# Kernel tuning notes

Hardware: AMD Instinct MI355X
Metric: run time of the kernel (lower is better)

The kernel has to match this reference:

```python
import jax, jax.numpy as jnp
import numpy as np

B, N, D_IN, D_SC, C, H, W = 32, 512, 256, 32, 48, 152, 160


def setup_inputs() -> dict:
    key = jax.random.key(0)
    k1, k2, k3, k4 = jax.random.split(key, 4)
    spatial_info = jax.random.normal(k1, (B, C, H, W), dtype=jnp.float32)
    entity_embeddings = jax.random.normal(k2, (B, N, D_IN), dtype=jnp.float32)
    entity_mask = jnp.ones((B, N), dtype=jnp.float32)
    locations = jax.random.randint(k3, (B, N, 2), 0, 152).astype(jnp.int64)
    W_proj = jax.random.normal(k4, (D_IN, D_SC), dtype=jnp.float32) / np.sqrt(D_IN)
    b_proj = jnp.zeros((D_SC,), dtype=jnp.float32)
    return {"spatial_info": spatial_info, "entity_embeddings": entity_embeddings,
            "entity_mask": entity_mask, "locations": locations,
            "W_proj": W_proj, "b_proj": b_proj}


def reference(spatial_info, entity_embeddings, entity_mask, locations, W_proj, b_proj):
    # fc_block: linear + ReLU projection of entity embeddings -> [B, N, D_SC]
    proj = jax.nn.relu(jnp.einsum('bnd,de->bne', entity_embeddings, W_proj) + b_proj)
    proj = proj * entity_mask[:, :, None]

    # build flat spatial indices (clamped), with per-batch bias  -> [B*N]
    y = jnp.clip(locations[..., 0], 0, H - 1)
    x = jnp.clip(locations[..., 1], 0, W - 1)
    flat = y * W + x                                   # [B, N]
    bias = (jnp.arange(B, dtype=flat.dtype) * (H * W))[:, None]
    idx = (flat + bias).reshape(-1)                    # [B*N]

    # scatter-add projected embeddings onto dense grid [B*H*W, D_SC]
    vals = proj.reshape(B * N, D_SC)
    scatter_map = jnp.zeros((B * H * W, D_SC), dtype=proj.dtype).at[idx].add(vals)
    scatter_map = scatter_map.reshape(B, H, W, D_SC).transpose(0, 3, 1, 2)  # [B, D_SC, H, W]

    return jnp.concatenate([spatial_info, scatter_map], axis=1)
```

## Files before the change

kernel.cpp:

```cpp
#include <hip/hip_runtime.h>

#define Bsz  32
#define Nn   512
#define DIN  256
#define DSC  32
#define Cc   48
#define Hh   152
#define Ww   160
#define HW   (Hh * Ww)
#define COUT (Cc + DSC)
#define HALF (HW / 2)
#define HP4  (HALF / 4)

#define CP_N4     (Bsz * Cc * (HW / 4))
#define CP_GRID   2048
#define CP_THREAD 256
#define CP_STRIDE (CP_GRID * CP_THREAD)
#define SLAB4     (Cc * (HW / 4))
#define SC4       ((COUT - Cc) * (HW / 4))
#define PR_GRID   ((Bsz * Nn) / 32)

typedef float f4 __attribute__((ext_vector_type(4)));

__global__ __launch_bounds__(CP_THREAD, 4) void proj_copy_kernel(
    const float* __restrict__ spatial, const float* __restrict__ emb,
    const float* __restrict__ mask, const int* __restrict__ loc,
    const float* __restrict__ Wp, const float* __restrict__ bp,
    float* __restrict__ out, float* __restrict__ projws,
    int* __restrict__ idxws) {

    __shared__ float Ws[DIN][DSC];

    const int bid = blockIdx.x;
    const int tid = threadIdx.x;

    if (bid >= PR_GRID) {
        const f4* __restrict__ src = (const f4*)spatial;
        f4* __restrict__       dst = (f4*)out;
        unsigned i = (bid - PR_GRID) * CP_THREAD + tid;
        #pragma unroll 1
        for (int k = 0; k < 4; ++k) {
            const unsigned i0 = i, i1 = i + CP_STRIDE,
                           i2 = i + 2 * CP_STRIDE, i3 = i + 3 * CP_STRIDE;
            const f4 a0 = src[i0];
            const f4 a1 = src[i1];
            const f4 a2 = src[i2];
            const f4 a3 = src[i3];
            __builtin_nontemporal_store(a0, dst + i0 + (i0 / (unsigned)SLAB4) * SC4);
            __builtin_nontemporal_store(a1, dst + i1 + (i1 / (unsigned)SLAB4) * SC4);
            __builtin_nontemporal_store(a2, dst + i2 + (i2 / (unsigned)SLAB4) * SC4);
            __builtin_nontemporal_store(a3, dst + i3 + (i3 / (unsigned)SLAB4) * SC4);
            i += 4 * CP_STRIDE;
        }
        {
            const f4 a = src[i];
            __builtin_nontemporal_store(a, dst + i + (i / (unsigned)SLAB4) * SC4);
            i += CP_STRIDE;
        }
        if (i < (unsigned)CP_N4) {
            const f4 a = src[i];
            __builtin_nontemporal_store(a, dst + i + (i / (unsigned)SLAB4) * SC4);
        }
        return;
    }

    const int ent0 = bid * 32;

    for (int i = tid; i < (DIN * DSC) / 4; i += 256)
        ((f4*)Ws)[i] = ((const f4*)Wp)[i];
    __syncthreads();

    const int g   = tid >> 3;
    const int dq  = (tid & 7) * 4;
    const int ent = ent0 + g;

    const f4* __restrict__ erow = (const f4*)(emb + (size_t)ent * DIN);

    float ax = bp[dq + 0], ay = bp[dq + 1], az = bp[dq + 2], aw = bp[dq + 3];

    #pragma unroll 4
    for (int k4 = 0; k4 < DIN / 4; ++k4) {
        const f4 ev = erow[k4];
        const int k = k4 * 4;
        const f4 w0 = *(const f4*)&Ws[k + 0][dq];
        const f4 w1 = *(const f4*)&Ws[k + 1][dq];
        const f4 w2 = *(const f4*)&Ws[k + 2][dq];
        const f4 w3 = *(const f4*)&Ws[k + 3][dq];
        ax = fmaf(ev.x, w0.x, fmaf(ev.y, w1.x, fmaf(ev.z, w2.x, fmaf(ev.w, w3.x, ax))));
        ay = fmaf(ev.x, w0.y, fmaf(ev.y, w1.y, fmaf(ev.z, w2.y, fmaf(ev.w, w3.y, ay))));
        az = fmaf(ev.x, w0.z, fmaf(ev.y, w1.z, fmaf(ev.z, w2.z, fmaf(ev.w, w3.z, az))));
        aw = fmaf(ev.x, w0.w, fmaf(ev.y, w1.w, fmaf(ev.z, w2.w, fmaf(ev.w, w3.w, aw))));
    }

    const float m = mask[ent];
    f4 r;
    r.x = fmaxf(ax, 0.f) * m;
    r.y = fmaxf(ay, 0.f) * m;
    r.z = fmaxf(az, 0.f) * m;
    r.w = fmaxf(aw, 0.f) * m;
    ((f4*)projws)[(size_t)ent * (DSC / 4) + (tid & 7)] = r;

    if ((tid & 7) == 0) {
        int y = loc[2 * ent + 0];
        int x = loc[2 * ent + 1];
        y = min(max(y, 0), Hh - 1);
        x = min(max(x, 0), Ww - 1);
        idxws[ent] = y * Ww + x;
    }
}

__global__ __launch_bounds__(256) void gather_kernel(
    const float* __restrict__ projws, const int* __restrict__ idxws,
    float* __restrict__ out) {

    __shared__ float facc[HALF];

    const int g    = blockIdx.x;
    const int b    = g >> 6;
    const int c    = (g >> 1) & 31;
    const int lo   = (g & 1) * HALF;
    const int tid  = threadIdx.x;

    for (int i = tid; i < HP4; i += 256) ((f4*)facc)[i] = (f4)(0.f);
    __syncthreads();

    const int2 v = ((const int2*)(idxws + b * Nn))[tid];
    {
        const int r0 = v.x - lo;
        if ((unsigned)r0 < (unsigned)HALF) {
            const float p = projws[((size_t)b * Nn + 2 * tid) * DSC + c];
            if (p != 0.f) atomicAdd(&facc[r0], p);
        }
        const int r1 = v.y - lo;
        if ((unsigned)r1 < (unsigned)HALF) {
            const float p = projws[((size_t)b * Nn + 2 * tid + 1) * DSC + c];
            if (p != 0.f) atomicAdd(&facc[r1], p);
        }
    }
    __syncthreads();

    f4* obase = (f4*)(out + ((size_t)(b * COUT + Cc + c)) * HW + lo);
    for (int i = tid; i < HP4; i += 256)
        __builtin_nontemporal_store(((const f4*)facc)[i], obase + i);
}

__global__ __launch_bounds__(256) void init_out_kernel(
    const float* __restrict__ spatial, float* __restrict__ out) {
    const int plane = blockIdx.x;
    const int b = plane / COUT;
    const int c = plane % COUT;
    f4* dst = (f4*)(out + (size_t)plane * HW);
    if (c < Cc) {
        const f4* src = (const f4*)(spatial + ((size_t)b * Cc + c) * HW);
        for (int i = threadIdx.x; i < HW / 4; i += blockDim.x) dst[i] = src[i];
    } else {
        for (int i = threadIdx.x; i < HW / 4; i += blockDim.x) dst[i] = (f4)(0.f);
    }
}

__global__ __launch_bounds__(256) void scatter_kernel(
    const float* __restrict__ emb, const float* __restrict__ mask,
    const int* __restrict__ loc, const float* __restrict__ Wp,
    const float* __restrict__ bp, float* __restrict__ out) {

    __shared__ float Ws[DIN][DSC];
    __shared__ float Es[32][DIN + 4];

    const int tid  = threadIdx.x;
    const int ent0 = blockIdx.x * 32;

    for (int i = tid; i < (DIN * DSC) / 4; i += 256)
        ((f4*)Ws)[i] = ((const f4*)Wp)[i];
    for (int i = tid; i < (32 * DIN) / 4; i += 256) {
        const int e  = i >> 6;
        const int k4 = i & 63;
        *(f4*)&Es[e][k4 * 4] =
            ((const f4*)(emb + (size_t)(ent0 + e) * DIN))[k4];
    }
    __syncthreads();

    const int g   = tid >> 3;
    const int dq  = (tid & 7) * 4;
    const int ent = ent0 + g;
    const int b   = ent >> 9;

    float ax = bp[dq + 0], ay = bp[dq + 1], az = bp[dq + 2], aw = bp[dq + 3];

    #pragma unroll 4
    for (int k = 0; k < DIN; k += 4) {
        const f4 ev = *(const f4*)&Es[g][k];
        const f4 w0 = *(const f4*)&Ws[k + 0][dq];
        const f4 w1 = *(const f4*)&Ws[k + 1][dq];
        const f4 w2 = *(const f4*)&Ws[k + 2][dq];
        const f4 w3 = *(const f4*)&Ws[k + 3][dq];
        ax = fmaf(ev.x, w0.x, fmaf(ev.y, w1.x, fmaf(ev.z, w2.x, fmaf(ev.w, w3.x, ax))));
        ay = fmaf(ev.x, w0.y, fmaf(ev.y, w1.y, fmaf(ev.z, w2.y, fmaf(ev.w, w3.y, ay))));
        az = fmaf(ev.x, w0.z, fmaf(ev.y, w1.z, fmaf(ev.z, w2.z, fmaf(ev.w, w3.z, az))));
        aw = fmaf(ev.x, w0.w, fmaf(ev.y, w1.w, fmaf(ev.z, w2.w, fmaf(ev.w, w3.w, aw))));
    }

    const float m = mask[ent];
    int y = loc[2 * ent + 0];
    int x = loc[2 * ent + 1];
    y = min(max(y, 0), Hh - 1);
    x = min(max(x, 0), Ww - 1);

    float* dst = out + ((size_t)b * COUT + Cc) * HW + (size_t)y * Ww + x;
    float v[4] = { ax, ay, az, aw };
    #pragma unroll
    for (int j = 0; j < 4; ++j) {
        const float r = fmaxf(v[j], 0.f) * m;
        if (r != 0.f)
            atomicAdd(dst + (size_t)(dq + j) * HW, r);
    }
}

extern "C" void kernel_launch(void* const* d_in, const int* in_sizes, int n_in,
                              void* d_out, int out_size, void* d_ws, size_t ws_size,
                              hipStream_t stream) {
    const float* spatial = (const float*)d_in[0];
    const float* emb     = (const float*)d_in[1];
    const float* mask    = (const float*)d_in[2];
    const int*   loc     = (const int*)d_in[3];
    const float* Wp      = (const float*)d_in[4];
    const float* bp      = (const float*)d_in[5];
    float* out = (float*)d_out;

    const size_t need = (size_t)Bsz * Nn * DSC * sizeof(float)
                      + (size_t)Bsz * Nn * sizeof(int);
    if (ws_size >= need) {
        float* projws = (float*)d_ws;
        int*   idxws  = (int*)((char*)d_ws + (size_t)Bsz * Nn * DSC * sizeof(float));
        proj_copy_kernel<<<PR_GRID + CP_GRID, CP_THREAD, 0, stream>>>(
            spatial, emb, mask, loc, Wp, bp, out, projws, idxws);
        gather_kernel<<<Bsz * DSC * 2, 256, 0, stream>>>(projws, idxws, out);
    } else {
        init_out_kernel<<<Bsz * COUT, 256, 0, stream>>>(spatial, out);
        scatter_kernel<<<(Bsz * Nn) / 32, 256, 0, stream>>>(emb, mask, loc, Wp, bp, out);
    }
}
```

Measured before the change: 71.53 us.

## Move spatial copy into gather kernel and make projection a standalone kernel

The projection now runs in its own small kernel that reads W directly from global memory/cache instead of staging it in LDS. The bulk spatial copy moves into the gather launch, with even and odd blocks interleaved so the bandwidth-bound copy overlaps the LDS-atomic gather rather than the projection. Since CP_GRID equals GA_GRID, the interleaving is an exact 1:1 split. The cost is that the copy now starts only after the projection kernel finishes, and the projection may be limited by global W loads.

After: 91.47 us. +27.9%, slower.

```diff
diff --git a/kernel.cpp b/kernel.cpp
--- a/kernel.cpp
+++ b/kernel.cpp
@@ -19,25 +19,71 @@
 #define SLAB4     (Cc * (HW / 4))
 #define SC4       ((COUT - Cc) * (HW / 4))
 #define PR_GRID   ((Bsz * Nn) / 32)
+#define GA_GRID   (Bsz * DSC * 2)
 
 typedef float f4 __attribute__((ext_vector_type(4)));
 
-__global__ __launch_bounds__(CP_THREAD, 4) void proj_copy_kernel(
-    const float* __restrict__ spatial, const float* __restrict__ emb,
-    const float* __restrict__ mask, const int* __restrict__ loc,
-    const float* __restrict__ Wp, const float* __restrict__ bp,
-    float* __restrict__ out, float* __restrict__ projws,
+__global__ __launch_bounds__(256) void proj_kernel(
+    const float* __restrict__ emb, const float* __restrict__ mask,
+    const int* __restrict__ loc, const float* __restrict__ Wp,
+    const float* __restrict__ bp, float* __restrict__ projws,
     int* __restrict__ idxws) {
 
-    __shared__ float Ws[DIN][DSC];
+    const int tid  = threadIdx.x;
+    const int g    = tid >> 3;
+    const int dq4  = tid & 7;
+    const int ent  = blockIdx.x * 32 + g;
+
+    const f4* __restrict__ erow = (const f4*)(emb + (size_t)ent * DIN);
+    const f4* __restrict__ wf4  = (const f4*)Wp;
+
+    const f4 bv = ((const f4*)bp)[dq4];
+    float ax = bv.x, ay = bv.y, az = bv.z, aw = bv.w;
+
+    #pragma unroll 4
+    for (int k4 = 0; k4 < DIN / 4; ++k4) {
+        const f4 ev = erow[k4];
+        const int k = k4 * 4;
+        const f4 w0 = wf4[(k + 0) * 8 + dq4];
+        const f4 w1 = wf4[(k + 1) * 8 + dq4];
+        const f4 w2 = wf4[(k + 2) * 8 + dq4];
+        const f4 w3 = wf4[(k + 3) * 8 + dq4];
+        ax = fmaf(ev.x, w0.x, fmaf(ev.y, w1.x, fmaf(ev.z, w2.x, fmaf(ev.w, w3.x, ax))));
+        ay = fmaf(ev.x, w0.y, fmaf(ev.y, w1.y, fmaf(ev.z, w2.y, fmaf(ev.w, w3.y, ay))));
+        az = fmaf(ev.x, w0.z, fmaf(ev.y, w1.z, fmaf(ev.z, w2.z, fmaf(ev.w, w3.z, az))));
+        aw = fmaf(ev.x, w0.w, fmaf(ev.y, w1.w, fmaf(ev.z, w2.w, fmaf(ev.w, w3.w, aw))));
+    }
+
+    const float m = mask[ent];
+    f4 r;
+    r.x = fmaxf(ax, 0.f) * m;
+    r.y = fmaxf(ay, 0.f) * m;
+    r.z = fmaxf(az, 0.f) * m;
+    r.w = fmaxf(aw, 0.f) * m;
+    ((f4*)projws)[(size_t)ent * (DSC / 4) + dq4] = r;
+
+    if (dq4 == 0) {
+        int y = loc[2 * ent + 0];
+        int x = loc[2 * ent + 1];
+        y = min(max(y, 0), Hh - 1);
+        x = min(max(x, 0), Ww - 1);
+        idxws[ent] = y * Ww + x;
+    }
+}
+
+__global__ __launch_bounds__(256) void copy_gather_kernel(
+    const float* __restrict__ spatial, const float* __restrict__ projws,
+    const int* __restrict__ idxws, float* __restrict__ out) {
+
+    __shared__ float facc[HALF];
 
     const int bid = blockIdx.x;
     const int tid = threadIdx.x;
 
-    if (bid >= PR_GRID) {
+    if ((bid & 1) == 0) {
         const f4* __restrict__ src = (const f4*)spatial;
         f4* __restrict__       dst = (f4*)out;
-        unsigned i = (bid - PR_GRID) * CP_THREAD + tid;
+        unsigned i = (unsigned)(bid >> 1) * CP_THREAD + tid;
         #pragma unroll 1
         for (int k = 0; k < 4; ++k) {
             const unsigned i0 = i, i1 = i + CP_STRIDE,
@@ -64,62 +110,10 @@
         return;
     }
 
-    const int ent0 = bid * 32;
-
-    for (int i = tid; i < (DIN * DSC) / 4; i += 256)
-        ((f4*)Ws)[i] = ((const f4*)Wp)[i];
-    __syncthreads();
-
-    const int g   = tid >> 3;
-    const int dq  = (tid & 7) * 4;
-    const int ent = ent0 + g;
-
-    const f4* __restrict__ erow = (const f4*)(emb + (size_t)ent * DIN);
-
-    float ax = bp[dq + 0], ay = bp[dq + 1], az = bp[dq + 2], aw = bp[dq + 3];
-
-    #pragma unroll 4
-    for (int k4 = 0; k4 < DIN / 4; ++k4) {
-        const f4 ev = erow[k4];
-        const int k = k4 * 4;
-        const f4 w0 = *(const f4*)&Ws[k + 0][dq];
-        const f4 w1 = *(const f4*)&Ws[k + 1][dq];
-        const f4 w2 = *(const f4*)&Ws[k + 2][dq];
-        const f4 w3 = *(const f4*)&Ws[k + 3][dq];
-        ax = fmaf(ev.x, w0.x, fmaf(ev.y, w1.x, fmaf(ev.z, w2.x, fmaf(ev.w, w3.x, ax))));
-        ay = fmaf(ev.x, w0.y, fmaf(ev.y, w1.y, fmaf(ev.z, w2.y, fmaf(ev.w, w3.y, ay))));
-        az = fmaf(ev.x, w0.z, fmaf(ev.y, w1.z, fmaf(ev.z, w2.z, fmaf(ev.w, w3.z, az))));
-        aw = fmaf(ev.x, w0.w, fmaf(ev.y, w1.w, fmaf(ev.z, w2.w, fmaf(ev.w, w3.w, aw))));
-    }
-
-    const float m = mask[ent];
-    f4 r;
-    r.x = fmaxf(ax, 0.f) * m;
-    r.y = fmaxf(ay, 0.f) * m;
-    r.z = fmaxf(az, 0.f) * m;
-    r.w = fmaxf(aw, 0.f) * m;
-    ((f4*)projws)[(size_t)ent * (DSC / 4) + (tid & 7)] = r;
-
-    if ((tid & 7) == 0) {
-        int y = loc[2 * ent + 0];
-        int x = loc[2 * ent + 1];
-        y = min(max(y, 0), Hh - 1);
-        x = min(max(x, 0), Ww - 1);
-        idxws[ent] = y * Ww + x;
-    }
-}
-
-__global__ __launch_bounds__(256) void gather_kernel(
-    const float* __restrict__ projws, const int* __restrict__ idxws,
-    float* __restrict__ out) {
-
-    __shared__ float facc[HALF];
-
-    const int g    = blockIdx.x;
-    const int b    = g >> 6;
-    const int c    = (g >> 1) & 31;
-    const int lo   = (g & 1) * HALF;
-    const int tid  = threadIdx.x;
+    const int gid = bid >> 1;
+    const int b   = gid >> 6;
+    const int c   = (gid >> 1) & 31;
+    const int lo  = (gid & 1) * HALF;
 
     for (int i = tid; i < HP4; i += 256) ((f4*)facc)[i] = (f4)(0.f);
     __syncthreads();
@@ -231,9 +225,10 @@
     if (ws_size >= need) {
         float* projws = (float*)d_ws;
         int*   idxws  = (int*)((char*)d_ws + (size_t)Bsz * Nn * DSC * sizeof(float));
-        proj_copy_kernel<<<PR_GRID + CP_GRID, CP_THREAD, 0, stream>>>(
-            spatial, emb, mask, loc, Wp, bp, out, projws, idxws);
-        gather_kernel<<<Bsz * DSC * 2, 256, 0, stream>>>(projws, idxws, out);
+        proj_kernel<<<PR_GRID, 256, 0, stream>>>(emb, mask, loc, Wp, bp,
+                                                 projws, idxws);
+        copy_gather_kernel<<<CP_GRID + GA_GRID, CP_THREAD, 0, stream>>>(
+            spatial, projws, idxws, out);
     } else {
         init_out_kernel<<<Bsz * COUT, 256, 0, stream>>>(spatial, out);
         scatter_kernel<<<(Bsz * Nn) / 32, 256, 0, stream>>>(emb, mask, loc, Wp, bp, out);
```
